# Optimization experiments

Measured on AMD Instinct MI355X. Metric: run time of the kernel, lower is better.

The kernel has to match this reference:

```python
import jax, jax.numpy as jnp
import numpy as np

N = 100000   # nodes
E = 1200000  # edges
B = 128      # graphs per batch
F = 92       # raw node features
D = 64       # pre_hidden_size == gc_dim == post_hidden_size
L = 3        # n_gcn
Z = 2 * D + 1  # CGConv concat width


def setup_inputs() -> dict:
    key = jax.random.key(0)
    ks = jax.random.split(key, 24)
    s = 0.1
    inp = {
        "X": jax.random.normal(ks[0], (N, F), jnp.float32),
        "edge_idx": jax.random.randint(ks[1], (2, E), 0, N),
        "edge_weight": jax.random.uniform(ks[2], (E,), jnp.float32),
        "edge_attr": jax.random.normal(ks[3], (E,), jnp.float32),
        "batch_map": jnp.sort(jax.random.randint(ks[4], (N,), 0, B)),
        # pre-GCN MLP: F->D, D->D, D->D, relu after each
        "pre_W0": jax.random.normal(ks[5], (F, D)) * s,
        "pre_b0": jnp.zeros((D,), jnp.float32),
        "pre_W1": jax.random.normal(ks[6], (D, D)) * s,
        "pre_b1": jnp.zeros((D,), jnp.float32),
        "pre_W2": jax.random.normal(ks[7], (D, D)) * s,
        "pre_b2": jnp.zeros((D,), jnp.float32),
        # CGConv gates: lin_f / lin_s: (2D+1)->D, stacked over L layers
        "cg_Wf": jax.random.normal(ks[8], (L, Z, D)) * s,
        "cg_bf": jnp.zeros((L, D), jnp.float32),
        "cg_Ws": jax.random.normal(ks[9], (L, Z, D)) * s,
        "cg_bs": jnp.zeros((L, D), jnp.float32),
        # post-GCN MLP: D->D x3 (relu) then D->1
        "post_W0": jax.random.normal(ks[10], (D, D)) * s,
        "post_b0": jnp.zeros((D,), jnp.float32),
        "post_W1": jax.random.normal(ks[11], (D, D)) * s,
        "post_b1": jnp.zeros((D,), jnp.float32),
        "post_W2": jax.random.normal(ks[12], (D, D)) * s,
        "post_b2": jnp.zeros((D,), jnp.float32),
        "post_Wf": jax.random.normal(ks[13], (D, 1)) * s,
        "post_bf": jnp.zeros((1,), jnp.float32),
    }
    return inp


def _forward(X, edge_idx, edge_weight, edge_attr, batch_map,
             pre_W0, pre_b0, pre_W1, pre_b1, pre_W2, pre_b2,
             cg_Wf, cg_bf, cg_Ws, cg_bs,
             post_W0, post_b0, post_W1, post_b1, post_W2, post_b2,
             post_Wf, post_bf):
    relu = jax.nn.relu
    # pre-GC MLP
    h = relu(X @ pre_W0 + pre_b0)
    h = relu(h @ pre_W1 + pre_b1)
    h = relu(h @ pre_W2 + pre_b2)  # [N, D]

    src = edge_idx[0]  # x_j (message source)
    dst = edge_idx[1]  # x_i (aggregation target)
    ea = edge_attr.reshape(-1, 1)  # [E, 1]
    # in-degree for mean aggregation (nodes with no edges -> 0 via denom clamp)
    deg = jax.ops.segment_sum(jnp.ones((E,), h.dtype), dst, num_segments=N)
    denom = jnp.maximum(deg, 1.0)[:, None]  # [N, 1]

    for l in range(L):
        # CGConv: z = [x_i || x_j || e], out = x + mean_i(sigmoid(z Wf) * softplus(z Ws))
        z = jnp.concatenate([h[dst], h[src], ea], axis=-1)  # [E, 2D+1]
        m = jax.nn.sigmoid(z @ cg_Wf[l] + cg_bf[l]) * jax.nn.softplus(z @ cg_Ws[l] + cg_bs[l])
        agg = jax.ops.segment_sum(m, dst, num_segments=N) / denom
        h = relu(h + agg)  # residual + activation from pyg Sequential

    # early global mean pool per graph
    gsum = jax.ops.segment_sum(h, batch_map, num_segments=B)
    gcnt = jax.ops.segment_sum(jnp.ones((N,), h.dtype), batch_map, num_segments=B)
    g = gsum / jnp.maximum(gcnt, 1.0)[:, None]  # [B, D]

    # post-GC MLP
    g = relu(g @ post_W0 + post_b0)
    g = relu(g @ post_W1 + post_b1)
    g = relu(g @ post_W2 + post_b2)
    return g @ post_Wf + post_bf  # [B, 1]


def reference(X, edge_idx, edge_weight, edge_attr, batch_map,
              pre_W0, pre_b0, pre_W1, pre_b1, pre_W2, pre_b2,
              cg_Wf, cg_bf, cg_Ws, cg_bs,
              post_W0, post_b0, post_W1, post_b1, post_W2, post_b2,
              post_Wf, post_bf):
    return _forward(X, edge_idx, edge_weight, edge_attr, batch_map,
                    pre_W0, pre_b0, pre_W1, pre_b1, pre_W2, pre_b2,
                    cg_Wf, cg_bf, cg_Ws, cg_bs,
                    post_W0, post_b0, post_W1, post_b1, post_W2, post_b2,
                    post_Wf, post_bf)
```

## Files before the change

kernel.cpp:

```cpp
#include <hip/hip_runtime.h>
#include <hip/hip_bf16.h>
#include <math.h>

#define GN 100000
#define GE 1200000
#define GB 128
#define GF 92
#define GD 64
#define GL 3
#define GZ 129

#define HS 65

__device__ __forceinline__ unsigned int f2bf_rne(float x)
{
    unsigned int u = __float_as_uint(x);
    u += 0x7fffu + ((u >> 16) & 1u);
    return u >> 16;
}

__global__ __launch_bounds__(256, 2) void premlp_kernel(
    const float* __restrict__ X,
    const float* __restrict__ W0, const float* __restrict__ b0,
    const float* __restrict__ W1, const float* __restrict__ b1,
    const float* __restrict__ W2, const float* __restrict__ b2,
    const float* __restrict__ WfD, const float* __restrict__ WsD,
    const float* __restrict__ WfS, const float* __restrict__ WsS,
    const float* __restrict__ bf, const float* __restrict__ bs,
    float* __restrict__ hout, unsigned int* __restrict__ Pout,
    float* __restrict__ Qout, int N)
{
    __shared__ __align__(16) float Wl[5888];
    __shared__ float hl[128 * HS];
    const int tid = threadIdx.x;
    const int lane = tid & 63;
    const int col0 = (tid >> 6) * 16;
    const int base = blockIdx.x * 128;
    const int n0 = base + lane;
    const int n1 = base + 64 + lane;
    const int nn0 = (n0 < N) ? n0 : (N - 1);
    const int nn1 = (n1 < N) ? n1 : (N - 1);
    const bool act0 = (n0 < N), act1 = (n1 < N);

    float a0[16], a1[16], s0[16], s1[16];

    {
        const float4* __restrict__ s4 = (const float4*)W0;
        float4* __restrict__ d4 = (float4*)Wl;
        for (int i = tid; i < 1472; i += 256) d4[i] = s4[i];
    }
    __syncthreads();

#pragma unroll
    for (int j = 0; j < 16; ++j) { a0[j] = b0[col0 + j]; a1[j] = a0[j]; }
    {
        const float4* __restrict__ r40 = (const float4*)(X + (size_t)nn0 * GF);
        const float4* __restrict__ r41 = (const float4*)(X + (size_t)nn1 * GF);
        for (int c = 0; c < 23; ++c) {
            float4 v0 = r40[c];
            float4 v1 = r41[c];
            const float* __restrict__ w = Wl + c * 256 + col0;
#pragma unroll
            for (int j = 0; j < 16; ++j) {
                float wa = w[j], wb = w[64 + j], wc = w[128 + j], wd = w[192 + j];
                a0[j] = fmaf(v0.x, wa, a0[j]);
                a0[j] = fmaf(v0.y, wb, a0[j]);
                a0[j] = fmaf(v0.z, wc, a0[j]);
                a0[j] = fmaf(v0.w, wd, a0[j]);
                a1[j] = fmaf(v1.x, wa, a1[j]);
                a1[j] = fmaf(v1.y, wb, a1[j]);
                a1[j] = fmaf(v1.z, wc, a1[j]);
                a1[j] = fmaf(v1.w, wd, a1[j]);
            }
        }
    }
    __syncthreads();
#pragma unroll
    for (int j = 0; j < 16; ++j) {
        hl[lane * HS + col0 + j] = fmaxf(a0[j], 0.f);
        hl[(64 + lane) * HS + col0 + j] = fmaxf(a1[j], 0.f);
    }
    {
        const float4* __restrict__ s4 = (const float4*)W1;
        float4* __restrict__ d4 = (float4*)Wl;
        for (int i = tid; i < 1024; i += 256) d4[i] = s4[i];
    }
    __syncthreads();

#pragma unroll
    for (int j = 0; j < 16; ++j) { a0[j] = b1[col0 + j]; a1[j] = a0[j]; }
    for (int c = 0; c < 16; ++c) {
        float h0 = hl[lane * HS + 4 * c + 0];
        float h1 = hl[lane * HS + 4 * c + 1];
        float h2 = hl[lane * HS + 4 * c + 2];
        float h3 = hl[lane * HS + 4 * c + 3];
        float g0 = hl[(64 + lane) * HS + 4 * c + 0];
        float g1 = hl[(64 + lane) * HS + 4 * c + 1];
        float g2 = hl[(64 + lane) * HS + 4 * c + 2];
        float g3 = hl[(64 + lane) * HS + 4 * c + 3];
        const float* __restrict__ w = Wl + c * 256 + col0;
#pragma unroll
        for (int j = 0; j < 16; ++j) {
            float wa = w[j], wb = w[64 + j], wc = w[128 + j], wd = w[192 + j];
            a0[j] = fmaf(h0, wa, a0[j]);
            a0[j] = fmaf(h1, wb, a0[j]);
            a0[j] = fmaf(h2, wc, a0[j]);
            a0[j] = fmaf(h3, wd, a0[j]);
            a1[j] = fmaf(g0, wa, a1[j]);
            a1[j] = fmaf(g1, wb, a1[j]);
            a1[j] = fmaf(g2, wc, a1[j]);
            a1[j] = fmaf(g3, wd, a1[j]);
        }
    }
    __syncthreads();
#pragma unroll
    for (int j = 0; j < 16; ++j) {
        hl[lane * HS + col0 + j] = fmaxf(a0[j], 0.f);
        hl[(64 + lane) * HS + col0 + j] = fmaxf(a1[j], 0.f);
    }
    {
        const float4* __restrict__ s4 = (const float4*)W2;
        float4* __restrict__ d4 = (float4*)Wl;
        for (int i = tid; i < 1024; i += 256) d4[i] = s4[i];
    }
    __syncthreads();

#pragma unroll
    for (int j = 0; j < 16; ++j) { a0[j] = b2[col0 + j]; a1[j] = a0[j]; }
    for (int c = 0; c < 16; ++c) {
        float h0 = hl[lane * HS + 4 * c + 0];
        float h1 = hl[lane * HS + 4 * c + 1];
        float h2 = hl[lane * HS + 4 * c + 2];
        float h3 = hl[lane * HS + 4 * c + 3];
        float g0 = hl[(64 + lane) * HS + 4 * c + 0];
        float g1 = hl[(64 + lane) * HS + 4 * c + 1];
        float g2 = hl[(64 + lane) * HS + 4 * c + 2];
        float g3 = hl[(64 + lane) * HS + 4 * c + 3];
        const float* __restrict__ w = Wl + c * 256 + col0;
#pragma unroll
        for (int j = 0; j < 16; ++j) {
            float wa = w[j], wb = w[64 + j], wc = w[128 + j], wd = w[192 + j];
            a0[j] = fmaf(h0, wa, a0[j]);
            a0[j] = fmaf(h1, wb, a0[j]);
            a0[j] = fmaf(h2, wc, a0[j]);
            a0[j] = fmaf(h3, wd, a0[j]);
            a1[j] = fmaf(g0, wa, a1[j]);
            a1[j] = fmaf(g1, wb, a1[j]);
            a1[j] = fmaf(g2, wc, a1[j]);
            a1[j] = fmaf(g3, wd, a1[j]);
        }
    }
    __syncthreads();
#pragma unroll
    for (int j = 0; j < 16; ++j) {
        hl[lane * HS + col0 + j] = fmaxf(a0[j], 0.f);
        hl[(64 + lane) * HS + col0 + j] = fmaxf(a1[j], 0.f);
    }
    if (act0) {
        float4* __restrict__ op = (float4*)(hout + (size_t)n0 * 64 + col0);
#pragma unroll
        for (int q = 0; q < 4; ++q)
            op[q] = make_float4(fmaxf(a0[q * 4], 0.f), fmaxf(a0[q * 4 + 1], 0.f),
                                fmaxf(a0[q * 4 + 2], 0.f), fmaxf(a0[q * 4 + 3], 0.f));
    }
    if (act1) {
        float4* __restrict__ op = (float4*)(hout + (size_t)n1 * 64 + col0);
#pragma unroll
        for (int q = 0; q < 4; ++q)
            op[q] = make_float4(fmaxf(a1[q * 4], 0.f), fmaxf(a1[q * 4 + 1], 0.f),
                                fmaxf(a1[q * 4 + 2], 0.f), fmaxf(a1[q * 4 + 3], 0.f));
    }
    {
        const float4* __restrict__ s4 = (const float4*)WfS;
        float4* __restrict__ d4 = (float4*)Wl;
        for (int i = tid; i < 1024; i += 256) d4[i] = s4[i];
    }
    __syncthreads();

#pragma unroll
    for (int j = 0; j < 16; ++j) { a0[j] = 0.f; a1[j] = 0.f; }
    for (int c = 0; c < 16; ++c) {
        float h0 = hl[lane * HS + 4 * c + 0];
        float h1 = hl[lane * HS + 4 * c + 1];
        float h2 = hl[lane * HS + 4 * c + 2];
        float h3 = hl[lane * HS + 4 * c + 3];
        float g0 = hl[(64 + lane) * HS + 4 * c + 0];
        float g1 = hl[(64 + lane) * HS + 4 * c + 1];
        float g2 = hl[(64 + lane) * HS + 4 * c + 2];
        float g3 = hl[(64 + lane) * HS + 4 * c + 3];
        const float* __restrict__ w = Wl + c * 256 + col0;
#pragma unroll
        for (int j = 0; j < 16; ++j) {
            float wa = w[j], wb = w[64 + j], wc = w[128 + j], wd = w[192 + j];
            a0[j] = fmaf(h0, wa, a0[j]);
            a0[j] = fmaf(h1, wb, a0[j]);
            a0[j] = fmaf(h2, wc, a0[j]);
            a0[j] = fmaf(h3, wd, a0[j]);
            a1[j] = fmaf(g0, wa, a1[j]);
            a1[j] = fmaf(g1, wb, a1[j]);
            a1[j] = fmaf(g2, wc, a1[j]);
            a1[j] = fmaf(g3, wd, a1[j]);
        }
    }
    __syncthreads();
    {
        const float4* __restrict__ s4 = (const float4*)WsS;
        float4* __restrict__ d4 = (float4*)Wl;
        for (int i = tid; i < 1024; i += 256) d4[i] = s4[i];
    }
    __syncthreads();

#pragma unroll
    for (int j = 0; j < 16; ++j) { s0[j] = 0.f; s1[j] = 0.f; }
    for (int c = 0; c < 16; ++c) {
        float h0 = hl[lane * HS + 4 * c + 0];
        float h1 = hl[lane * HS + 4 * c + 1];
        float h2 = hl[lane * HS + 4 * c + 2];
        float h3 = hl[lane * HS + 4 * c + 3];
        float g0 = hl[(64 + lane) * HS + 4 * c + 0];
        float g1 = hl[(64 + lane) * HS + 4 * c + 1];
        float g2 = hl[(64 + lane) * HS + 4 * c + 2];
        float g3 = hl[(64 + lane) * HS + 4 * c + 3];
        const float* __restrict__ w = Wl + c * 256 + col0;
#pragma unroll
        for (int j = 0; j < 16; ++j) {
            float wa = w[j], wb = w[64 + j], wc = w[128 + j], wd = w[192 + j];
            s0[j] = fmaf(h0, wa, s0[j]);
            s0[j] = fmaf(h1, wb, s0[j]);
            s0[j] = fmaf(h2, wc, s0[j]);
            s0[j] = fmaf(h3, wd, s0[j]);
            s1[j] = fmaf(g0, wa, s1[j]);
            s1[j] = fmaf(g1, wb, s1[j]);
            s1[j] = fmaf(g2, wc, s1[j]);
            s1[j] = fmaf(g3, wd, s1[j]);
        }
    }
    if (act0) {
        uint4* __restrict__ pp = (uint4*)(Pout + (size_t)n0 * 64 + col0);
#pragma unroll
        for (int q = 0; q < 4; ++q) {
            uint4 pk;
            pk.x = f2bf_rne(a0[q * 4])     | (f2bf_rne(s0[q * 4]) << 16);
            pk.y = f2bf_rne(a0[q * 4 + 1]) | (f2bf_rne(s0[q * 4 + 1]) << 16);
            pk.z = f2bf_rne(a0[q * 4 + 2]) | (f2bf_rne(s0[q * 4 + 2]) << 16);
            pk.w = f2bf_rne(a0[q * 4 + 3]) | (f2bf_rne(s0[q * 4 + 3]) << 16);
            pp[q] = pk;
        }
    }
    if (act1) {
        uint4* __restrict__ pp = (uint4*)(Pout + (size_t)n1 * 64 + col0);
#pragma unroll
        for (int q = 0; q < 4; ++q) {
            uint4 pk;
            pk.x = f2bf_rne(a1[q * 4])     | (f2bf_rne(s1[q * 4]) << 16);
            pk.y = f2bf_rne(a1[q * 4 + 1]) | (f2bf_rne(s1[q * 4 + 1]) << 16);
            pk.z = f2bf_rne(a1[q * 4 + 2]) | (f2bf_rne(s1[q * 4 + 2]) << 16);
            pk.w = f2bf_rne(a1[q * 4 + 3]) | (f2bf_rne(s1[q * 4 + 3]) << 16);
            pp[q] = pk;
        }
    }
    __syncthreads();
    {
        const float4* __restrict__ s4 = (const float4*)WfD;
        float4* __restrict__ d4 = (float4*)Wl;
        for (int i = tid; i < 1024; i += 256) d4[i] = s4[i];
    }
    __syncthreads();

#pragma unroll
    for (int j = 0; j < 16; ++j) { a0[j] = bf[col0 + j]; a1[j] = a0[j]; }
    for (int c = 0; c < 16; ++c) {
        float h0 = hl[lane * HS + 4 * c + 0];
        float h1 = hl[lane * HS + 4 * c + 1];
        float h2 = hl[lane * HS + 4 * c + 2];
        float h3 = hl[lane * HS + 4 * c + 3];
        float g0 = hl[(64 + lane) * HS + 4 * c + 0];
        float g1 = hl[(64 + lane) * HS + 4 * c + 1];
        float g2 = hl[(64 + lane) * HS + 4 * c + 2];
        float g3 = hl[(64 + lane) * HS + 4 * c + 3];
        const float* __restrict__ w = Wl + c * 256 + col0;
#pragma unroll
        for (int j = 0; j < 16; ++j) {
            float wa = w[j], wb = w[64 + j], wc = w[128 + j], wd = w[192 + j];
            a0[j] = fmaf(h0, wa, a0[j]);
            a0[j] = fmaf(h1, wb, a0[j]);
            a0[j] = fmaf(h2, wc, a0[j]);
            a0[j] = fmaf(h3, wd, a0[j]);
            a1[j] = fmaf(g0, wa, a1[j]);
            a1[j] = fmaf(g1, wb, a1[j]);
            a1[j] = fmaf(g2, wc, a1[j]);
            a1[j] = fmaf(g3, wd, a1[j]);
        }
    }
    __syncthreads();
    {
        const float4* __restrict__ s4 = (const float4*)WsD;
        float4* __restrict__ d4 = (float4*)Wl;
        for (int i = tid; i < 1024; i += 256) d4[i] = s4[i];
    }
    __syncthreads();

#pragma unroll
    for (int j = 0; j < 16; ++j) { s0[j] = bs[col0 + j]; s1[j] = s0[j]; }
    for (int c = 0; c < 16; ++c) {
        float h0 = hl[lane * HS + 4 * c + 0];
        float h1 = hl[lane * HS + 4 * c + 1];
        float h2 = hl[lane * HS + 4 * c + 2];
        float h3 = hl[lane * HS + 4 * c + 3];
        float g0 = hl[(64 + lane) * HS + 4 * c + 0];
        float g1 = hl[(64 + lane) * HS + 4 * c + 1];
        float g2 = hl[(64 + lane) * HS + 4 * c + 2];
        float g3 = hl[(64 + lane) * HS + 4 * c + 3];
        const float* __restrict__ w = Wl + c * 256 + col0;
#pragma unroll
        for (int j = 0; j < 16; ++j) {
            float wa = w[j], wb = w[64 + j], wc = w[128 + j], wd = w[192 + j];
            s0[j] = fmaf(h0, wa, s0[j]);
            s0[j] = fmaf(h1, wb, s0[j]);
            s0[j] = fmaf(h2, wc, s0[j]);
            s0[j] = fmaf(h3, wd, s0[j]);
            s1[j] = fmaf(g0, wa, s1[j]);
            s1[j] = fmaf(g1, wb, s1[j]);
            s1[j] = fmaf(g2, wc, s1[j]);
            s1[j] = fmaf(g3, wd, s1[j]);
        }
    }
    if (act0) {
        float4* __restrict__ qp = (float4*)(Qout + (size_t)n0 * 128 + col0 * 2);
#pragma unroll
        for (int q = 0; q < 8; ++q)
            qp[q] = make_float4(a0[q * 2], s0[q * 2], a0[q * 2 + 1], s0[q * 2 + 1]);
    }
    if (act1) {
        float4* __restrict__ qp = (float4*)(Qout + (size_t)n1 * 128 + col0 * 2);
#pragma unroll
        for (int q = 0; q < 8; ++q)
            qp[q] = make_float4(a1[q * 2], s1[q * 2], a1[q * 2 + 1], s1[q * 2 + 1]);
    }
}

__global__ __launch_bounds__(256, 3) void pjq_kernel(
    const float* __restrict__ h,
    const float* __restrict__ Wf, const float* __restrict__ Ws,
    const float* __restrict__ bfv, const float* __restrict__ bsv,
    unsigned int* __restrict__ P, float* __restrict__ Q, int N)
{
    __shared__ __align__(16) float Wl[8192];
    const int tid = threadIdx.x;
    const int lane = tid & 63;
    const int col0 = (tid >> 6) * 16;
    const int base = blockIdx.x * 128;
    const int n0 = base + lane;
    const int n1 = base + 64 + lane;
    const int nn0 = (n0 < N) ? n0 : (N - 1);
    const int nn1 = (n1 < N) ? n1 : (N - 1);
    const bool act0 = (n0 < N), act1 = (n1 < N);

    const float4* __restrict__ h40 = (const float4*)(h + (size_t)nn0 * 64);
    const float4* __restrict__ h41 = (const float4*)(h + (size_t)nn1 * 64);

    float aF0[16], aF1[16], aS0[16], aS1[16];

    {
        const float4* __restrict__ f4 = (const float4*)(Wf + 64 * 64);
        const float4* __restrict__ s4 = (const float4*)(Ws + 64 * 64);
        float4* __restrict__ d4 = (float4*)Wl;
        for (int i = tid; i < 1024; i += 256) {
            d4[i] = f4[i];
            d4[1024 + i] = s4[i];
        }
    }
    __syncthreads();

#pragma unroll
    for (int j = 0; j < 16; ++j) { aF0[j] = 0.f; aF1[j] = 0.f; aS0[j] = 0.f; aS1[j] = 0.f; }
    for (int c = 0; c < 16; ++c) {
        float4 v0 = h40[c];
        float4 v1 = h41[c];
        const float* __restrict__ wf = Wl + c * 256 + col0;
        const float* __restrict__ ws = Wl + 4096 + c * 256 + col0;
#pragma unroll
        for (int j = 0; j < 16; ++j) {
            float wa = wf[j], wb = wf[64 + j], wc = wf[128 + j], wd = wf[192 + j];
            aF0[j] = fmaf(v0.x, wa, aF0[j]);
            aF0[j] = fmaf(v0.y, wb, aF0[j]);
            aF0[j] = fmaf(v0.z, wc, aF0[j]);
            aF0[j] = fmaf(v0.w, wd, aF0[j]);
            aF1[j] = fmaf(v1.x, wa, aF1[j]);
            aF1[j] = fmaf(v1.y, wb, aF1[j]);
            aF1[j] = fmaf(v1.z, wc, aF1[j]);
            aF1[j] = fmaf(v1.w, wd, aF1[j]);
            float sa = ws[j], sb = ws[64 + j], sc = ws[128 + j], sd = ws[192 + j];
            aS0[j] = fmaf(v0.x, sa, aS0[j]);
            aS0[j] = fmaf(v0.y, sb, aS0[j]);
            aS0[j] = fmaf(v0.z, sc, aS0[j]);
            aS0[j] = fmaf(v0.w, sd, aS0[j]);
            aS1[j] = fmaf(v1.x, sa, aS1[j]);
            aS1[j] = fmaf(v1.y, sb, aS1[j]);
            aS1[j] = fmaf(v1.z, sc, aS1[j]);
            aS1[j] = fmaf(v1.w, sd, aS1[j]);
        }
    }
    if (act0) {
        uint4* __restrict__ pp = (uint4*)(P + (size_t)n0 * 64 + col0);
#pragma unroll
        for (int q = 0; q < 4; ++q) {
            uint4 pk;
            pk.x = f2bf_rne(aF0[q * 4])     | (f2bf_rne(aS0[q * 4]) << 16);
            pk.y = f2bf_rne(aF0[q * 4 + 1]) | (f2bf_rne(aS0[q * 4 + 1]) << 16);
            pk.z = f2bf_rne(aF0[q * 4 + 2]) | (f2bf_rne(aS0[q * 4 + 2]) << 16);
            pk.w = f2bf_rne(aF0[q * 4 + 3]) | (f2bf_rne(aS0[q * 4 + 3]) << 16);
            pp[q] = pk;
        }
    }
    if (act1) {
        uint4* __restrict__ pp = (uint4*)(P + (size_t)n1 * 64 + col0);
#pragma unroll
        for (int q = 0; q < 4; ++q) {
            uint4 pk;
            pk.x = f2bf_rne(aF1[q * 4])     | (f2bf_rne(aS1[q * 4]) << 16);
            pk.y = f2bf_rne(aF1[q * 4 + 1]) | (f2bf_rne(aS1[q * 4 + 1]) << 16);
            pk.z = f2bf_rne(aF1[q * 4 + 2]) | (f2bf_rne(aS1[q * 4 + 2]) << 16);
            pk.w = f2bf_rne(aF1[q * 4 + 3]) | (f2bf_rne(aS1[q * 4 + 3]) << 16);
            pp[q] = pk;
        }
    }
    __syncthreads();

    {
        const float4* __restrict__ f4 = (const float4*)Wf;
        const float4* __restrict__ s4 = (const float4*)Ws;
        float4* __restrict__ d4 = (float4*)Wl;
        for (int i = tid; i < 1024; i += 256) {
            d4[i] = f4[i];
            d4[1024 + i] = s4[i];
        }
    }
    __syncthreads();

#pragma unroll
    for (int j = 0; j < 16; ++j) {
        aF0[j] = bfv[col0 + j]; aF1[j] = aF0[j];
        aS0[j] = bsv[col0 + j]; aS1[j] = aS0[j];
    }
    for (int c = 0; c < 16; ++c) {
        float4 v0 = h40[c];
        float4 v1 = h41[c];
        const float* __restrict__ wf = Wl + c * 256 + col0;
        const float* __restrict__ ws = Wl + 4096 + c * 256 + col0;
#pragma unroll
        for (int j = 0; j < 16; ++j) {
            float wa = wf[j], wb = wf[64 + j], wc = wf[128 + j], wd = wf[192 + j];
            aF0[j] = fmaf(v0.x, wa, aF0[j]);
            aF0[j] = fmaf(v0.y, wb, aF0[j]);
            aF0[j] = fmaf(v0.z, wc, aF0[j]);
            aF0[j] = fmaf(v0.w, wd, aF0[j]);
            aF1[j] = fmaf(v1.x, wa, aF1[j]);
            aF1[j] = fmaf(v1.y, wb, aF1[j]);
            aF1[j] = fmaf(v1.z, wc, aF1[j]);
            aF1[j] = fmaf(v1.w, wd, aF1[j]);
            float sa = ws[j], sb = ws[64 + j], sc = ws[128 + j], sd = ws[192 + j];
            aS0[j] = fmaf(v0.x, sa, aS0[j]);
            aS0[j] = fmaf(v0.y, sb, aS0[j]);
            aS0[j] = fmaf(v0.z, sc, aS0[j]);
            aS0[j] = fmaf(v0.w, sd, aS0[j]);
            aS1[j] = fmaf(v1.x, sa, aS1[j]);
            aS1[j] = fmaf(v1.y, sb, aS1[j]);
            aS1[j] = fmaf(v1.z, sc, aS1[j]);
            aS1[j] = fmaf(v1.w, sd, aS1[j]);
        }
    }
    if (act0) {
        float4* __restrict__ qp = (float4*)(Q + (size_t)n0 * 128 + col0 * 2);
#pragma unroll
        for (int q = 0; q < 8; ++q)
            qp[q] = make_float4(aF0[q * 2], aS0[q * 2], aF0[q * 2 + 1], aS0[q * 2 + 1]);
    }
    if (act1) {
        float4* __restrict__ qp = (float4*)(Q + (size_t)n1 * 128 + col0 * 2);
#pragma unroll
        for (int q = 0; q < 8; ++q)
            qp[q] = make_float4(aF1[q * 2], aS1[q * 2], aF1[q * 2 + 1], aS1[q * 2 + 1]);
    }
}

__global__ __launch_bounds__(256) void deg_kernel(
    const int* __restrict__ dst, int* __restrict__ deg, int E)
{
    int e = blockIdx.x * blockDim.x + threadIdx.x;
    if (e < E) atomicAdd(&deg[dst[e]], 1);
}

__global__ __launch_bounds__(1024) void scanA_kernel(
    const int* __restrict__ deg, int* __restrict__ iscan,
    int* __restrict__ bsum, int N)
{
    __shared__ int lds[1024];
    int tid = threadIdx.x;
    int gid = blockIdx.x * 1024 + tid;
    int v = (gid < N) ? deg[gid] : 0;
    lds[tid] = v; __syncthreads();
    for (int off = 1; off < 1024; off <<= 1) {
        int t = (tid >= off) ? lds[tid - off] : 0;
        __syncthreads();
        lds[tid] += t;
        __syncthreads();
    }
    if (gid < N) iscan[gid] = lds[tid];
    if (tid == 1023) bsum[blockIdx.x] = lds[1023];
}

__global__ __launch_bounds__(128) void scanB_kernel(
    const int* __restrict__ bsum, int* __restrict__ boff, int nb)
{
    __shared__ int lds[128];
    int t = threadIdx.x;
    int v = (t < nb) ? bsum[t] : 0;
    lds[t] = v; __syncthreads();
    for (int off = 1; off < 128; off <<= 1) {
        int u = (t >= off) ? lds[t - off] : 0;
        __syncthreads();
        lds[t] += u;
        __syncthreads();
    }
    if (t < nb) boff[t] = lds[t] - v;
}

__global__ __launch_bounds__(256) void scanC_kernel(
    const int* __restrict__ iscan, const int* __restrict__ boff,
    const int* __restrict__ deg,
    int* __restrict__ rowptr, int* __restrict__ cursor, int N)
{
    int i = blockIdx.x * blockDim.x + threadIdx.x;
    if (i >= N) return;
    int incl = iscan[i] + boff[i >> 10];
    rowptr[i + 1] = incl;
    cursor[i] = incl - deg[i];
    if (i == 0) rowptr[0] = 0;
}

__global__ __launch_bounds__(256) void escatter_kernel(
    const int* __restrict__ src, const int* __restrict__ dst,
    const float* __restrict__ ea, int* __restrict__ cursor,
    int2* __restrict__ e_se, int E)
{
    int e = blockIdx.x * blockDim.x + threadIdx.x;
    if (e >= E) return;
    int pos = atomicAdd(&cursor[dst[e]], 1);
    e_se[pos] = make_int2(src[e], __float_as_int(ea[e]));
}

__global__ __launch_bounds__(256) void edge_kernel(
    const float* __restrict__ h, const int* __restrict__ rowptr,
    const int2* __restrict__ e_se,
    const unsigned int* __restrict__ P,
    const float* __restrict__ Q,
    const float* __restrict__ Wf, const float* __restrict__ Ws,
    float* __restrict__ hout)
{
    int n = blockIdx.x * 4 + (threadIdx.x >> 6);
    int d = threadIdx.x & 63;

    const float2 qv = ((const float2*)Q)[(size_t)n * 64 + d];
    float qf = qv.x, qs = qv.y;
    float wf = Wf[128 * 64 + d];
    float ws = Ws[128 * 64 + d];

    size_t idx = (size_t)n * 64 + d;
    float hres = h[idx];

    int rb = rowptr[n], re = rowptr[n + 1];
    float agg = 0.f;
#pragma unroll 8
    for (int p = rb; p < re; ++p) {
        int2 se = e_se[p];
        int s = se.x;
        float ea = __int_as_float(se.y);
        unsigned int pv = P[(size_t)s * 64 + d];
        float pf = __uint_as_float(pv << 16);
        float psv = __uint_as_float(pv & 0xffff0000u);
        float xF = fmaf(ea, wf, qf + pf);
        float xS = fmaf(ea, ws, qs + psv);
        float sig = __builtin_amdgcn_rcpf(1.f + __expf(-xF));
        float t = __expf(-fabsf(xS));
        float sp = fmaxf(xS, 0.f) + __logf(1.f + t);
        agg = fmaf(sig, sp, agg);
    }

    float inv = 1.f / (float)max(re - rb, 1);
    hout[idx] = fmaxf(hres + agg * inv, 0.f);
}

__global__ __launch_bounds__(256) void gstart_kernel(
    const int* __restrict__ bm, int* __restrict__ gstart, int N)
{
    int i = blockIdx.x * blockDim.x + threadIdx.x;
    if (i >= N) return;
    int b = bm[i];
    int prev = (i == 0) ? -1 : bm[i - 1];
    for (int g = prev + 1; g <= b; ++g) gstart[g] = i;
    if (i == N - 1)
        for (int g = b + 1; g <= GB; ++g) gstart[g] = N;
}

__global__ __launch_bounds__(256) void pool_seg_kernel(
    const float* __restrict__ h, const int* __restrict__ gstart,
    float* __restrict__ g)
{
    int b = blockIdx.x;
    int s = gstart[b], e = gstart[b + 1];
    int d = threadIdx.x & 63;
    int w = threadIdx.x >> 6;
    float acc = 0.f;
    for (int n = s + w; n < e; n += 4)
        acc += h[(size_t)n * 64 + d];
    __shared__ float lds[256];
    lds[threadIdx.x] = acc;
    __syncthreads();
    if (w == 0) {
        acc = lds[d] + lds[64 + d] + lds[128 + d] + lds[192 + d];
        g[b * 64 + d] = acc / fmaxf((float)(e - s), 1.f);
    }
}

__global__ __launch_bounds__(256) void postmlp_kernel(
    const float* __restrict__ g,
    const float* __restrict__ W0, const float* __restrict__ b0,
    const float* __restrict__ W1, const float* __restrict__ b1,
    const float* __restrict__ W2, const float* __restrict__ b2,
    const float* __restrict__ Wfin, const float* __restrict__ bfin,
    float* __restrict__ out)
{
    int b = blockIdx.x * 4 + (threadIdx.x >> 6);
    int d = threadIdx.x & 63;
    float h = g[(size_t)b * 64 + d];

    float acc = b0[d];
#pragma unroll
    for (int k = 0; k < 64; ++k)
        acc = fmaf(__shfl(h, k, 64), W0[k * 64 + d], acc);
    h = fmaxf(acc, 0.f);

    acc = b1[d];
#pragma unroll
    for (int k = 0; k < 64; ++k)
        acc = fmaf(__shfl(h, k, 64), W1[k * 64 + d], acc);
    h = fmaxf(acc, 0.f);

    acc = b2[d];
#pragma unroll
    for (int k = 0; k < 64; ++k)
        acc = fmaf(__shfl(h, k, 64), W2[k * 64 + d], acc);
    h = fmaxf(acc, 0.f);

    float v = h * Wfin[d];
#pragma unroll
    for (int off = 32; off >= 1; off >>= 1)
        v += __shfl_xor(v, off, 64);
    if (d == 0) out[b] = v + bfin[0];
}

extern "C" void kernel_launch(void* const* d_in, const int* in_sizes, int n_in,
                              void* d_out, int out_size, void* d_ws, size_t ws_size,
                              hipStream_t stream)
{
    const float* X      = (const float*)d_in[0];
    const int*   eidx   = (const int*)d_in[1];
    const float* ea     = (const float*)d_in[3];
    const int*   bm     = (const int*)d_in[4];
    const float* pre_W0 = (const float*)d_in[5];
    const float* pre_b0 = (const float*)d_in[6];
    const float* pre_W1 = (const float*)d_in[7];
    const float* pre_b1 = (const float*)d_in[8];
    const float* pre_W2 = (const float*)d_in[9];
    const float* pre_b2 = (const float*)d_in[10];
    const float* cg_Wf  = (const float*)d_in[11];
    const float* cg_bf  = (const float*)d_in[12];
    const float* cg_Ws  = (const float*)d_in[13];
    const float* cg_bs  = (const float*)d_in[14];
    const float* post_W0 = (const float*)d_in[15];
    const float* post_b0 = (const float*)d_in[16];
    const float* post_W1 = (const float*)d_in[17];
    const float* post_b1 = (const float*)d_in[18];
    const float* post_W2 = (const float*)d_in[19];
    const float* post_b2 = (const float*)d_in[20];
    const float* post_Wf = (const float*)d_in[21];
    const float* post_bf = (const float*)d_in[22];

    const int* src = eidx;
    const int* dst = eidx + GE;

    const size_t N64 = (size_t)GN * 64;
    float* hA    = (float*)d_ws;
    float* hB    = hA + N64;
    unsigned int* P = (unsigned int*)(hB + N64);
    int* deg_i   = (int*)(P + N64);
    int* iscan   = deg_i + GN;
    int* bsum    = iscan + GN;
    int* boff    = bsum + 128;
    int* rowptr  = boff + 128;
    int* cursor  = rowptr + GN + 2;
    int2* e_se   = (int2*)(cursor + GN);
    int* gstart  = (int*)(e_se + GE);
    float* g0    = (float*)(gstart + GB + 1);
    float* Q     = g0 + (size_t)GB * 64;

    const int TPB = 256;
    int gridE  = (GE + TPB - 1) / TPB;
    int gridN  = (GN + TPB - 1) / TPB;
    int gridP  = (GN + 127) / 128;
    int gridND = ((GN * 64) + TPB - 1) / TPB;
    int scanBlocks = (GN + 1023) / 1024;

    const float* Wf0 = cg_Wf;
    const float* Ws0 = cg_Ws;
    const float* Wf1 = cg_Wf + (size_t)1 * GZ * GD;
    const float* Ws1 = cg_Ws + (size_t)1 * GZ * GD;
    const float* Wf2 = cg_Wf + (size_t)2 * GZ * GD;
    const float* Ws2 = cg_Ws + (size_t)2 * GZ * GD;

    premlp_kernel<<<gridP, TPB, 0, stream>>>(
        X, pre_W0, pre_b0, pre_W1, pre_b1, pre_W2, pre_b2,
        Wf0, Ws0, Wf0 + 64 * 64, Ws0 + 64 * 64, cg_bf, cg_bs,
        hA, P, Q, GN);

    hipMemsetAsync(deg_i, 0, GN * sizeof(int), stream);
    deg_kernel<<<gridE, TPB, 0, stream>>>(dst, deg_i, GE);
    scanA_kernel<<<scanBlocks, 1024, 0, stream>>>(deg_i, iscan, bsum, GN);
    scanB_kernel<<<1, 128, 0, stream>>>(bsum, boff, scanBlocks);
    scanC_kernel<<<gridN, TPB, 0, stream>>>(iscan, boff, deg_i, rowptr, cursor, GN);
    escatter_kernel<<<gridE, TPB, 0, stream>>>(src, dst, ea, cursor, e_se, GE);

    gstart_kernel<<<gridN, TPB, 0, stream>>>(bm, gstart, GN);

    edge_kernel<<<gridND, TPB, 0, stream>>>(
        hA, rowptr, e_se, P, Q, Wf0, Ws0, hB);
    pjq_kernel<<<gridP, TPB, 0, stream>>>(
        hB, Wf1, Ws1, cg_bf + GD, cg_bs + GD, P, Q, GN);
    edge_kernel<<<gridND, TPB, 0, stream>>>(
        hB, rowptr, e_se, P, Q, Wf1, Ws1, hA);
    pjq_kernel<<<gridP, TPB, 0, stream>>>(
        hA, Wf2, Ws2, cg_bf + 2 * GD, cg_bs + 2 * GD, P, Q, GN);
    edge_kernel<<<gridND, TPB, 0, stream>>>(
        hA, rowptr, e_se, P, Q, Wf2, Ws2, hB);

    pool_seg_kernel<<<GB, TPB, 0, stream>>>(hB, gstart, g0);

    postmlp_kernel<<<GB / 4, TPB, 0, stream>>>(
        g0, post_W0, post_b0, post_W1, post_b1, post_W2, post_b2,
        post_Wf, post_bf, (float*)d_out);
}
```

Baseline: 889.1 us.

## Restructure pjq kernel to keep weight columns in registers per lane

The per-node gate projection kernel now gives each lane one output column and keeps that column's 64 weights in registers, instead of staging weights in LDS with each thread computing 16 columns for two nodes. Each wavefront handles 32 nodes two at a time, reading h rows as wave-uniform broadcast loads. This drops the LDS traffic and block barriers, but it needs many registers, which may lower occupancy. It also changes the launch geometry from 128 nodes per block to 128 nodes per block split across four wavefronts.

```diff
diff --git a/kernel.cpp b/kernel.cpp
--- a/kernel.cpp
+++ b/kernel.cpp
@@ -345,142 +345,89 @@
     const float* __restrict__ bfv, const float* __restrict__ bsv,
     unsigned int* __restrict__ P, float* __restrict__ Q, int N)
 {
-    __shared__ __align__(16) float Wl[8192];
-    const int tid = threadIdx.x;
-    const int lane = tid & 63;
-    const int col0 = (tid >> 6) * 16;
-    const int base = blockIdx.x * 128;
-    const int n0 = base + lane;
-    const int n1 = base + 64 + lane;
-    const int nn0 = (n0 < N) ? n0 : (N - 1);
-    const int nn1 = (n1 < N) ? n1 : (N - 1);
-    const bool act0 = (n0 < N), act1 = (n1 < N);
-
-    const float4* __restrict__ h40 = (const float4*)(h + (size_t)nn0 * 64);
-    const float4* __restrict__ h41 = (const float4*)(h + (size_t)nn1 * 64);
-
-    float aF0[16], aF1[16], aS0[16], aS1[16];
-
-    {
-        const float4* __restrict__ f4 = (const float4*)(Wf + 64 * 64);
-        const float4* __restrict__ s4 = (const float4*)(Ws + 64 * 64);
-        float4* __restrict__ d4 = (float4*)Wl;
-        for (int i = tid; i < 1024; i += 256) {
-            d4[i] = f4[i];
-            d4[1024 + i] = s4[i];
-        }
-    }
-    __syncthreads();
-
-#pragma unroll
-    for (int j = 0; j < 16; ++j) { aF0[j] = 0.f; aF1[j] = 0.f; aS0[j] = 0.f; aS1[j] = 0.f; }
-    for (int c = 0; c < 16; ++c) {
-        float4 v0 = h40[c];
-        float4 v1 = h41[c];
-        const float* __restrict__ wf = Wl + c * 256 + col0;
-        const float* __restrict__ ws = Wl + 4096 + c * 256 + col0;
-#pragma unroll
-        for (int j = 0; j < 16; ++j) {
-            float wa = wf[j], wb = wf[64 + j], wc = wf[128 + j], wd = wf[192 + j];
-            aF0[j] = fmaf(v0.x, wa, aF0[j]);
-            aF0[j] = fmaf(v0.y, wb, aF0[j]);
-            aF0[j] = fmaf(v0.z, wc, aF0[j]);
-            aF0[j] = fmaf(v0.w, wd, aF0[j]);
-            aF1[j] = fmaf(v1.x, wa, aF1[j]);
-            aF1[j] = fmaf(v1.y, wb, aF1[j]);
-            aF1[j] = fmaf(v1.z, wc, aF1[j]);
-            aF1[j] = fmaf(v1.w, wd, aF1[j]);
-            float sa = ws[j], sb = ws[64 + j], sc = ws[128 + j], sd = ws[192 + j];
-            aS0[j] = fmaf(v0.x, sa, aS0[j]);
-            aS0[j] = fmaf(v0.y, sb, aS0[j]);
-            aS0[j] = fmaf(v0.z, sc, aS0[j]);
-            aS0[j] = fmaf(v0.w, sd, aS0[j]);
-            aS1[j] = fmaf(v1.x, sa, aS1[j]);
-            aS1[j] = fmaf(v1.y, sb, aS1[j]);
-            aS1[j] = fmaf(v1.z, sc, aS1[j]);
-            aS1[j] = fmaf(v1.w, sd, aS1[j]);
-        }
-    }
-    if (act0) {
-        uint4* __restrict__ pp = (uint4*)(P + (size_t)n0 * 64 + col0);
-#pragma unroll
-        for (int q = 0; q < 4; ++q) {
-            uint4 pk;
-            pk.x = f2bf_rne(aF0[q * 4])     | (f2bf_rne(aS0[q * 4]) << 16);
-            pk.y = f2bf_rne(aF0[q * 4 + 1]) | (f2bf_rne(aS0[q * 4 + 1]) << 16);
-            pk.z = f2bf_rne(aF0[q * 4 + 2]) | (f2bf_rne(aS0[q * 4 + 2]) << 16);
-            pk.w = f2bf_rne(aF0[q * 4 + 3]) | (f2bf_rne(aS0[q * 4 + 3]) << 16);
-            pp[q] = pk;
-        }
-    }
-    if (act1) {
-        uint4* __restrict__ pp = (uint4*)(P + (size_t)n1 * 64 + col0);
-#pragma unroll
-        for (int q = 0; q < 4; ++q) {
-            uint4 pk;
-            pk.x = f2bf_rne(aF1[q * 4])     | (f2bf_rne(aS1[q * 4]) << 16);
-            pk.y = f2bf_rne(aF1[q * 4 + 1]) | (f2bf_rne(aS1[q * 4 + 1]) << 16);
-            pk.z = f2bf_rne(aF1[q * 4 + 2]) | (f2bf_rne(aS1[q * 4 + 2]) << 16);
-            pk.w = f2bf_rne(aF1[q * 4 + 3]) | (f2bf_rne(aS1[q * 4 + 3]) << 16);
-            pp[q] = pk;
-        }
-    }
-    __syncthreads();
-
-    {
-        const float4* __restrict__ f4 = (const float4*)Wf;
-        const float4* __restrict__ s4 = (const float4*)Ws;
-        float4* __restrict__ d4 = (float4*)Wl;
-        for (int i = tid; i < 1024; i += 256) {
-            d4[i] = f4[i];
-            d4[1024 + i] = s4[i];
-        }
-    }
-    __syncthreads();
-
-#pragma unroll
-    for (int j = 0; j < 16; ++j) {
-        aF0[j] = bfv[col0 + j]; aF1[j] = aF0[j];
-        aS0[j] = bsv[col0 + j]; aS1[j] = aS0[j];
-    }
-    for (int c = 0; c < 16; ++c) {
-        float4 v0 = h40[c];
-        float4 v1 = h41[c];
-        const float* __restrict__ wf = Wl + c * 256 + col0;
-        const float* __restrict__ ws = Wl + 4096 + c * 256 + col0;
-#pragma unroll
-        for (int j = 0; j < 16; ++j) {
-            float wa = wf[j], wb = wf[64 + j], wc = wf[128 + j], wd = wf[192 + j];
-            aF0[j] = fmaf(v0.x, wa, aF0[j]);
-            aF0[j] = fmaf(v0.y, wb, aF0[j]);
-            aF0[j] = fmaf(v0.z, wc, aF0[j]);
-            aF0[j] = fmaf(v0.w, wd, aF0[j]);
-            aF1[j] = fmaf(v1.x, wa, aF1[j]);
-            aF1[j] = fmaf(v1.y, wb, aF1[j]);
-            aF1[j] = fmaf(v1.z, wc, aF1[j]);
-            aF1[j] = fmaf(v1.w, wd, aF1[j]);
-            float sa = ws[j], sb = ws[64 + j], sc = ws[128 + j], sd = ws[192 + j];
-            aS0[j] = fmaf(v0.x, sa, aS0[j]);
-            aS0[j] = fmaf(v0.y, sb, aS0[j]);
-            aS0[j] = fmaf(v0.z, sc, aS0[j]);
-            aS0[j] = fmaf(v0.w, sd, aS0[j]);
-            aS1[j] = fmaf(v1.x, sa, aS1[j]);
-            aS1[j] = fmaf(v1.y, sb, aS1[j]);
-            aS1[j] = fmaf(v1.z, sc, aS1[j]);
-            aS1[j] = fmaf(v1.w, sd, aS1[j]);
-        }
-    }
-    if (act0) {
-        float4* __restrict__ qp = (float4*)(Q + (size_t)n0 * 128 + col0 * 2);
-#pragma unroll
-        for (int q = 0; q < 8; ++q)
-            qp[q] = make_float4(aF0[q * 2], aS0[q * 2], aF0[q * 2 + 1], aS0[q * 2 + 1]);
-    }
-    if (act1) {
-        float4* __restrict__ qp = (float4*)(Q + (size_t)n1 * 128 + col0 * 2);
-#pragma unroll
-        for (int q = 0; q < 8; ++q)
-            qp[q] = make_float4(aF1[q * 2], aS1[q * 2], aF1[q * 2 + 1], aS1[q * 2 + 1]);
+    const int lane = threadIdx.x & 63;
+    const int wu = __builtin_amdgcn_readfirstlane((int)(threadIdx.x >> 6));
+    const int base = (blockIdx.x * 4 + wu) * 32;
+    if (base >= N) return;
+    const int nend = (base + 32 < N) ? base + 32 : N;
+
+    {
+        float wf[64], ws[64];
+#pragma unroll
+        for (int k = 0; k < 64; ++k) {
+            wf[k] = Wf[(64 + k) * 64 + lane];
+            ws[k] = Ws[(64 + k) * 64 + lane];
+        }
+        for (int n = base; n < nend; n += 2) {
+            const int m = (n + 1 < nend) ? n + 1 : n;
+            const float4* __restrict__ h0 = (const float4*)(h + (size_t)n * 64);
+            const float4* __restrict__ h1 = (const float4*)(h + (size_t)m * 64);
+            float f0 = 0.f, s0 = 0.f, f1 = 0.f, s1 = 0.f;
+#pragma unroll
+            for (int c = 0; c < 16; ++c) {
+                float4 v0 = h0[c];
+                float4 v1 = h1[c];
+                f0 = fmaf(v0.x, wf[4 * c + 0], f0);
+                f0 = fmaf(v0.y, wf[4 * c + 1], f0);
+                f0 = fmaf(v0.z, wf[4 * c + 2], f0);
+                f0 = fmaf(v0.w, wf[4 * c + 3], f0);
+                s0 = fmaf(v0.x, ws[4 * c + 0], s0);
+                s0 = fmaf(v0.y, ws[4 * c + 1], s0);
+                s0 = fmaf(v0.z, ws[4 * c + 2], s0);
+                s0 = fmaf(v0.w, ws[4 * c + 3], s0);
+                f1 = fmaf(v1.x, wf[4 * c + 0], f1);
+                f1 = fmaf(v1.y, wf[4 * c + 1], f1);
+                f1 = fmaf(v1.z, wf[4 * c + 2], f1);
+                f1 = fmaf(v1.w, wf[4 * c + 3], f1);
+                s1 = fmaf(v1.x, ws[4 * c + 0], s1);
+                s1 = fmaf(v1.y, ws[4 * c + 1], s1);
+                s1 = fmaf(v1.z, ws[4 * c + 2], s1);
+                s1 = fmaf(v1.w, ws[4 * c + 3], s1);
+            }
+            P[(size_t)n * 64 + lane] = f2bf_rne(f0) | (f2bf_rne(s0) << 16);
+            if (m > n)
+                P[(size_t)m * 64 + lane] = f2bf_rne(f1) | (f2bf_rne(s1) << 16);
+        }
+    }
+
+    {
+        float wf[64], ws[64];
+#pragma unroll
+        for (int k = 0; k < 64; ++k) {
+            wf[k] = Wf[k * 64 + lane];
+            ws[k] = Ws[k * 64 + lane];
+        }
+        const float bfj = bfv[lane], bsj = bsv[lane];
+        for (int n = base; n < nend; n += 2) {
+            const int m = (n + 1 < nend) ? n + 1 : n;
+            const float4* __restrict__ h0 = (const float4*)(h + (size_t)n * 64);
+            const float4* __restrict__ h1 = (const float4*)(h + (size_t)m * 64);
+            float f0 = bfj, s0 = bsj, f1 = bfj, s1 = bsj;
+#pragma unroll
+            for (int c = 0; c < 16; ++c) {
+                float4 v0 = h0[c];
+                float4 v1 = h1[c];
+                f0 = fmaf(v0.x, wf[4 * c + 0], f0);
+                f0 = fmaf(v0.y, wf[4 * c + 1], f0);
+                f0 = fmaf(v0.z, wf[4 * c + 2], f0);
+                f0 = fmaf(v0.w, wf[4 * c + 3], f0);
+                s0 = fmaf(v0.x, ws[4 * c + 0], s0);
+                s0 = fmaf(v0.y, ws[4 * c + 1], s0);
+                s0 = fmaf(v0.z, ws[4 * c + 2], s0);
+                s0 = fmaf(v0.w, ws[4 * c + 3], s0);
+                f1 = fmaf(v1.x, wf[4 * c + 0], f1);
+                f1 = fmaf(v1.y, wf[4 * c + 1], f1);
+                f1 = fmaf(v1.z, wf[4 * c + 2], f1);
+                f1 = fmaf(v1.w, wf[4 * c + 3], f1);
+                s1 = fmaf(v1.x, ws[4 * c + 0], s1);
+                s1 = fmaf(v1.y, ws[4 * c + 1], s1);
+                s1 = fmaf(v1.z, ws[4 * c + 2], s1);
+                s1 = fmaf(v1.w, ws[4 * c + 3], s1);
+            }
+            ((float2*)Q)[(size_t)n * 64 + lane] = make_float2(f0, s0);
+            if (m > n)
+                ((float2*)Q)[(size_t)m * 64 + lane] = make_float2(f1, s1);
+        }
     }
 }
 
```

Result: slower. 921.9 us (+3.7%).
